# Kernel tuning notes

Measured on AMD Instinct MI355X. Metric: run time of the kernel, lower is better.

## Reference

```python
import jax, jax.numpy as jnp
import numpy as np

DIM = 512
NUM_HEADS = 8
HEAD_DIM = DIM // NUM_HEADS
GAMMA = 1.0


def setup_inputs() -> dict:
    key = jax.random.key(0)
    ks = jax.random.split(key, 10)
    B, S = 2, 2048
    x_real = jax.random.normal(ks[0], (B, S, DIM), dtype=jnp.float32)
    x_imag = jax.random.normal(ks[1], (B, S, DIM), dtype=jnp.float32)
    def xavier(k, fan_in, fan_out):
        lim = float(np.sqrt(6.0 / (fan_in + fan_out)))
        return jax.random.uniform(k, (fan_in, fan_out), jnp.float32, -lim, lim)
    # torch Linear(in,out): weight [out,in]; we store transposed [in,out]
    Wq = xavier(ks[2], 2 * DIM, DIM); bq = jnp.zeros((DIM,), jnp.float32)
    Wk = xavier(ks[3], 2 * DIM, DIM); bk = jnp.zeros((DIM,), jnp.float32)
    Wv = xavier(ks[4], 2 * DIM, DIM); bv = jnp.zeros((DIM,), jnp.float32)
    Wo = xavier(ks[5], DIM, 2 * DIM); bo = jnp.zeros((2 * DIM,), jnp.float32)
    return {"x_real": x_real, "x_imag": x_imag, "Wq": Wq, "bq": bq,
            "Wk": Wk, "bk": bk, "Wv": Wv, "bv": bv, "Wo": Wo, "bo": bo}


def reference(x_real, x_imag, Wq, bq, Wk, bk, Wv, bv, Wo, bo):
    B, S, _ = x_real.shape
    real_embed = jnp.concatenate([x_real, x_imag], axis=-1)  # [B,S,2*dim]
    def proj(W, b):
        y = real_embed @ W + b                               # [B,S,dim]
        return y.reshape(B, S, NUM_HEADS, HEAD_DIM).transpose(0, 2, 1, 3)  # [B,H,S,d]
    Q = proj(Wq, bq)
    K = proj(Wk, bk)
    V = proj(Wv, bv)
    # softmax over head_dim is broadcast-invariant, so the Bhattacharyya
    # coefficient sum_d sqrt(p_i[d]*q_j[d]) factorizes into a matmul.
    sp = jnp.sqrt(jax.nn.softmax(Q, axis=-1))  # [B,H,S,d]
    sq = jnp.sqrt(jax.nn.softmax(K, axis=-1))  # [B,H,S,d]
    bc = jnp.einsum('bhid,bhjd->bhij', sp, sq)  # Bhattacharyya coeff [B,H,S,S]
    bc = jnp.clip(bc, -1.0, 1.0)
    dist = jnp.arccos(bc)
    attn = jax.nn.softmax(-GAMMA * dist * dist, axis=-1)  # [B,H,S,S]
    attended = jnp.einsum('bhij,bhjd->bhid', attn, V)
    attended = attended.transpose(0, 2, 1, 3).reshape(B, S, DIM)
    out = attended @ Wo + bo  # [B,S,2*dim] = concat(real_out, imag_out)
    return out
```

## Files before the change

kernel.cpp:

```cpp
#include <hip/hip_runtime.h>
#include <math.h>


typedef __attribute__((ext_vector_type(8))) short short8;
typedef __attribute__((ext_vector_type(4))) float f32x4;

#define MFMA(a, b, c) __builtin_amdgcn_mfma_f32_16x16x32_bf16((a), (b), (c), 0, 0, 0)

static __device__ __forceinline__ short f2bf(float f) {
    unsigned u = __float_as_uint(f);
    u += 0x7fffu + ((u >> 16) & 1u);
    return (short)(u >> 16);
}

__global__ __launch_bounds__(256) void convert_x(
    const float* __restrict__ xr, const float* __restrict__ xi,
    short* __restrict__ xb)
{
    int idx = blockIdx.x * 256 + threadIdx.x;
    int e = idx << 2;
    int m = e >> 10, k = e & 1023;
    const float* src = (k < 512) ? xr : xi;
    float4 t = *(const float4*)(src + (size_t)m * 512 + (k & 511));
    unsigned lo = (unsigned short)f2bf(t.x) | ((unsigned)(unsigned short)f2bf(t.y) << 16);
    unsigned hi = (unsigned short)f2bf(t.z) | ((unsigned)(unsigned short)f2bf(t.w) << 16);
    uint2 o; o.x = lo; o.y = hi;
    *(uint2*)(xb + e) = o;
}

__global__ __launch_bounds__(256) void transpose_w(
    const float* __restrict__ Wq, const float* __restrict__ Wk,
    const float* __restrict__ Wv, const float* __restrict__ Wo,
    short* __restrict__ wqt, short* __restrict__ wkt,
    short* __restrict__ wvt, short* __restrict__ wot)
{
    __shared__ float t[32][33];
    const int z = blockIdx.z;
    const float* src = (z == 0) ? Wq : (z == 1) ? Wk : (z == 2) ? Wv : Wo;
    short* dst = (z == 0) ? wqt : (z == 1) ? wkt : (z == 2) ? wvt : wot;
    const int K = (z < 3) ? 1024 : 512;
    const int N = (z < 3) ? 512 : 1024;
    const int n0 = blockIdx.x << 5, k0 = blockIdx.y << 5;
    if (n0 >= N || k0 >= K) return;
    const int tx = threadIdx.x & 31, ty = threadIdx.x >> 5;
    #pragma unroll
    for (int i = 0; i < 4; ++i)
        t[ty + 8 * i][tx] = src[(size_t)(k0 + ty + 8 * i) * N + n0 + tx];
    __syncthreads();
    #pragma unroll
    for (int i = 0; i < 4; ++i)
        dst[(size_t)(n0 + ty + 8 * i) * K + k0 + tx] = f2bf(t[tx][ty + 8 * i]);
}

__global__ __launch_bounds__(128) void qkv_mfma(
    const short* __restrict__ xb,
    const short* __restrict__ wqt, const short* __restrict__ wkt,
    const short* __restrict__ wvt,
    const float* __restrict__ bq, const float* __restrict__ bk,
    const float* __restrict__ bv,
    short* __restrict__ sp, short* __restrict__ sq, short* __restrict__ vt)
{
    __shared__ short vbuf[2][64 * 72];
    const int iwb = blockIdx.x;
    const int iw = iwb >> 3;
    const int h  = iwb & 7;
    const int tid = threadIdx.x;
    const int w = tid >> 6, lane = tid & 63;
    const int l = lane & 15, quad = lane >> 4;
    const int m0 = blockIdx.y * 128 + w * 64;

    const short* wt   = (iw == 0) ? wqt : (iw == 1) ? wkt : wvt;
    const float* bias = (iw == 0) ? bq  : (iw == 1) ? bk  : bv;
    short* dst        = (iw == 0) ? sp  : (iw == 1) ? sq  : vt;

    const short* ap[4];
    const short* bp[4];
    #pragma unroll
    for (int i = 0; i < 4; ++i)
        ap[i] = xb + (size_t)(m0 + i * 16 + l) * 1024 + quad * 8;
    #pragma unroll
    for (int j = 0; j < 4; ++j)
        bp[j] = wt + (size_t)(h * 64 + j * 16 + l) * 1024 + quad * 8;

    const f32x4 z4 = {0.f, 0.f, 0.f, 0.f};
    f32x4 acc[4][4];
    #pragma unroll
    for (int i = 0; i < 4; ++i)
        #pragma unroll
        for (int j = 0; j < 4; ++j) acc[i][j] = z4;

    short8 Af[4], Bf[4], Ag[4], Bg[4];
    #pragma unroll
    for (int i = 0; i < 4; ++i) { Af[i] = *(const short8*)ap[i]; Bf[i] = *(const short8*)bp[i]; }

    #pragma unroll 1
    for (int kc = 0; kc < 32; kc += 2) {
        const int ko1 = (kc + 1) * 32;
        #pragma unroll
        for (int i = 0; i < 4; ++i) {
            Ag[i] = *(const short8*)(ap[i] + ko1);
            Bg[i] = *(const short8*)(bp[i] + ko1);
        }
        #pragma unroll
        for (int i = 0; i < 4; ++i)
            #pragma unroll
            for (int j = 0; j < 4; ++j)
                acc[i][j] = MFMA(Af[i], Bf[j], acc[i][j]);
        const int ko2 = (kc + 2 < 32) ? (kc + 2) * 32 : 0;
        #pragma unroll
        for (int i = 0; i < 4; ++i) {
            Af[i] = *(const short8*)(ap[i] + ko2);
            Bf[i] = *(const short8*)(bp[i] + ko2);
        }
        #pragma unroll
        for (int i = 0; i < 4; ++i)
            #pragma unroll
            for (int j = 0; j < 4; ++j)
                acc[i][j] = MFMA(Ag[i], Bg[j], acc[i][j]);
    }

    float bcol[4];
    #pragma unroll
    for (int nt = 0; nt < 4; ++nt) bcol[nt] = bias[h * 64 + nt * 16 + l];

    #pragma unroll
    for (int i = 0; i < 4; ++i) {
        #pragma unroll
        for (int reg = 0; reg < 4; ++reg) {
            const int sg = m0 + i * 16 + quad * 4 + reg;
            const int b = sg >> 11, s = sg & 2047;
            float v[4];
            #pragma unroll
            for (int nt = 0; nt < 4; ++nt) v[nt] = acc[i][nt][reg] + bcol[nt];
            if (iw < 2) {
                float mx = fmaxf(fmaxf(v[0], v[1]), fmaxf(v[2], v[3]));
                #pragma unroll
                for (int msk = 1; msk < 16; msk <<= 1) mx = fmaxf(mx, __shfl_xor(mx, msk));
                float e[4], ssum = 0.f;
                #pragma unroll
                for (int nt = 0; nt < 4; ++nt) { e[nt] = __expf(v[nt] - mx); ssum += e[nt]; }
                #pragma unroll
                for (int msk = 1; msk < 16; msk <<= 1) ssum += __shfl_xor(ssum, msk);
                float inv = 1.0f / ssum;
                short* o = dst + ((size_t)(b * 8 + h) * 2048 + s) * 64 + l;
                #pragma unroll
                for (int nt = 0; nt < 4; ++nt)
                    o[nt * 16] = f2bf(sqrtf(e[nt] * inv));
            } else {
                const int sl = i * 16 + quad * 4 + reg;
                #pragma unroll
                for (int nt = 0; nt < 4; ++nt)
                    vbuf[w][(nt * 16 + l) * 72 + sl] = f2bf(v[nt]);
            }
        }
    }

    if (iw == 2) {
        const int d = lane;
        const short* row = &vbuf[w][d * 72];
        const int b = m0 >> 11, s0 = m0 & 2047;
        short* gp = vt + ((size_t)(b * 8 + h) * 64 + d) * 2048 + s0;
        #pragma unroll
        for (int r = 0; r < 8; ++r)
            *(short8*)(gp + r * 8) = *(const short8*)(row + r * 8);
    }
}

__global__ __launch_bounds__(256, 4) void attn_mfma(
    const short* __restrict__ sp, const short* __restrict__ sq,
    const short* __restrict__ vt, short* __restrict__ attB)
{
    __shared__ short sqT[2][64 * 72];
    __shared__ short vtT[2][64 * 72];
    __shared__ short Pb[4][16 * 72];
    __shared__ float denB[4][16];
    const int bh = blockIdx.y;
    const int m0 = blockIdx.x << 6;
    const int tid = threadIdx.x;
    const int w = tid >> 6, lane = tid & 63;
    const int l = lane & 15, quad = lane >> 4;

    const short* spB = sp + (size_t)bh * 2048 * 64;
    const short* sqB = sq + (size_t)bh * 2048 * 64;
    const short* vtB = vt + (size_t)bh * 64 * 2048;

    const short* apr = spB + (size_t)(m0 + w * 16 + l) * 64 + quad * 8;
    short8 aq0 = *(const short8*)(apr);
    short8 aq1 = *(const short8*)(apr + 32);

    const int srow = tid >> 2;
    const int scol = (tid & 3) * 16;
    const short* sqG = sqB + (size_t)srow * 64 + scol;
    const short* vtG = vtB + (size_t)srow * 2048 + scol;
    const int ldsOff = srow * 72 + scol;

    {
        short8 a0 = *(const short8*)(sqG);
        short8 a1 = *(const short8*)(sqG + 8);
        short8 b0 = *(const short8*)(vtG);
        short8 b1 = *(const short8*)(vtG + 8);
        *(short8*)(&sqT[0][ldsOff])     = a0;
        *(short8*)(&sqT[0][ldsOff + 8]) = a1;
        *(short8*)(&vtT[0][ldsOff])     = b0;
        *(short8*)(&vtT[0][ldsOff + 8]) = b1;
    }
    __syncthreads();

    const f32x4 z4 = {0.f, 0.f, 0.f, 0.f};
    f32x4 acc[4] = {z4, z4, z4, z4};
    float den = 0.f;
    short* Pw = &Pb[w][0];

    #pragma unroll 1
    for (int jt = 0; jt < 32; ++jt) {
        const int cb = jt & 1, nb = cb ^ 1;
        const int j0n = ((jt + 1) & 31) << 6;
        short8 na0 = *(const short8*)(sqG + (size_t)j0n * 64);
        short8 na1 = *(const short8*)(sqG + (size_t)j0n * 64 + 8);
        short8 nb0 = *(const short8*)(vtG + j0n);
        short8 nb1 = *(const short8*)(vtG + j0n + 8);

        const short* sqL = &sqT[cb][0];
        #pragma unroll
        for (int nt = 0; nt < 4; ++nt) {
            const short* ar = sqL + (nt * 16 + l) * 72 + quad * 8;
            short8 sa0 = *(const short8*)(ar);
            short8 sa1 = *(const short8*)(ar + 32);
            f32x4 p = MFMA(sa0, aq0, z4);
            p = MFMA(sa1, aq1, p);
            float wv[4];
            #pragma unroll
            for (int reg = 0; reg < 4; ++reg) {
                float u = fmaxf(1.0f - p[reg], 0.0f);
                float t = 0.000922f;
                t = fmaf(t, u, 0.00152228f);
                t = fmaf(t, u, 0.00384801f);
                t = fmaf(t, u, 0.01015873f);
                t = fmaf(t, u, 0.02857143f);
                t = fmaf(t, u, 0.08888889f);
                t = fmaf(t, u, 0.33333333f);
                t = fmaf(t, u, 2.0f);
                float e = __expf(-u * t);
                wv[reg] = e;
                den += e;
            }
            uint2 pk;
            pk.x = (__float_as_uint(wv[0]) >> 16) | (__float_as_uint(wv[1]) & 0xffff0000u);
            pk.y = (__float_as_uint(wv[2]) >> 16) | (__float_as_uint(wv[3]) & 0xffff0000u);
            *(uint2*)(&Pw[l * 72 + nt * 16 + quad * 4]) = pk;
        }

        const short* pr = Pw + l * 72 + quad * 8;
        short8 pa0 = *(const short8*)(pr);
        short8 pa1 = *(const short8*)(pr + 32);
        const short* vL = &vtT[cb][0];
        #pragma unroll
        for (int t4 = 0; t4 < 4; ++t4) {
            const short* vr = vL + (t4 * 16 + l) * 72 + quad * 8;
            short8 vb0 = *(const short8*)(vr);
            short8 vb1 = *(const short8*)(vr + 32);
            acc[t4] = MFMA(pa0, vb0, acc[t4]);
            acc[t4] = MFMA(pa1, vb1, acc[t4]);
        }

        *(short8*)(&sqT[nb][ldsOff])     = na0;
        *(short8*)(&sqT[nb][ldsOff + 8]) = na1;
        *(short8*)(&vtT[nb][ldsOff])     = nb0;
        *(short8*)(&vtT[nb][ldsOff + 8]) = nb1;
        __syncthreads();
    }

    den += __shfl_xor(den, 16);
    den += __shfl_xor(den, 32);
    if (lane < 16) denB[w][l] = den;
    float invd[4];
    #pragma unroll
    for (int reg = 0; reg < 4; ++reg)
        invd[reg] = 1.0f / denB[w][quad * 4 + reg];

    const int b = bh >> 3, hh = bh & 7;
    #pragma unroll
    for (int t4 = 0; t4 < 4; ++t4)
        #pragma unroll
        for (int reg = 0; reg < 4; ++reg) {
            const int row = m0 + w * 16 + quad * 4 + reg;
            attB[((size_t)(b * 2048 + row)) * 512 + hh * 64 + t4 * 16 + l] =
                f2bf(acc[t4][reg] * invd[reg]);
        }
}

__global__ __launch_bounds__(128) void out_mfma(
    const short* __restrict__ attB, const short* __restrict__ wot,
    const float* __restrict__ bo, float* __restrict__ out)
{
    const int n0 = blockIdx.x << 6;
    const int tid = threadIdx.x;
    const int w = tid >> 6, lane = tid & 63;
    const int l = lane & 15, quad = lane >> 4;
    const int m0 = blockIdx.y * 128 + w * 64;

    const short* ap[4];
    const short* bp[4];
    #pragma unroll
    for (int i = 0; i < 4; ++i)
        ap[i] = attB + (size_t)(m0 + i * 16 + l) * 512 + quad * 8;
    #pragma unroll
    for (int j = 0; j < 4; ++j)
        bp[j] = wot + (size_t)(n0 + j * 16 + l) * 512 + quad * 8;

    const f32x4 z4 = {0.f, 0.f, 0.f, 0.f};
    f32x4 acc[4][4];
    #pragma unroll
    for (int i = 0; i < 4; ++i)
        #pragma unroll
        for (int j = 0; j < 4; ++j) acc[i][j] = z4;

    short8 Af[4], Bf[4], Ag[4], Bg[4];
    #pragma unroll
    for (int i = 0; i < 4; ++i) { Af[i] = *(const short8*)ap[i]; Bf[i] = *(const short8*)bp[i]; }

    #pragma unroll 1
    for (int kc = 0; kc < 16; kc += 2) {
        const int ko1 = (kc + 1) * 32;
        #pragma unroll
        for (int i = 0; i < 4; ++i) {
            Ag[i] = *(const short8*)(ap[i] + ko1);
            Bg[i] = *(const short8*)(bp[i] + ko1);
        }
        #pragma unroll
        for (int i = 0; i < 4; ++i)
            #pragma unroll
            for (int j = 0; j < 4; ++j)
                acc[i][j] = MFMA(Af[i], Bf[j], acc[i][j]);
        const int ko2 = (kc + 2 < 16) ? (kc + 2) * 32 : 0;
        #pragma unroll
        for (int i = 0; i < 4; ++i) {
            Af[i] = *(const short8*)(ap[i] + ko2);
            Bf[i] = *(const short8*)(bp[i] + ko2);
        }
        #pragma unroll
        for (int i = 0; i < 4; ++i)
            #pragma unroll
            for (int j = 0; j < 4; ++j)
                acc[i][j] = MFMA(Ag[i], Bg[j], acc[i][j]);
    }

    #pragma unroll
    for (int i = 0; i < 4; ++i)
        #pragma unroll
        for (int reg = 0; reg < 4; ++reg) {
            const int m = m0 + i * 16 + quad * 4 + reg;
            float* o = out + (size_t)m * 1024 + n0 + l;
            #pragma unroll
            for (int nt = 0; nt < 4; ++nt)
                o[nt * 16] = acc[i][nt][reg] + bo[n0 + nt * 16 + l];
        }
}

extern "C" void kernel_launch(void* const* d_in, const int* in_sizes, int n_in,
                              void* d_out, int out_size, void* d_ws, size_t ws_size,
                              hipStream_t stream) {
    const float* xr = (const float*)d_in[0];
    const float* xi = (const float*)d_in[1];
    const float* Wq = (const float*)d_in[2];
    const float* bq = (const float*)d_in[3];
    const float* Wk = (const float*)d_in[4];
    const float* bk = (const float*)d_in[5];
    const float* Wv = (const float*)d_in[6];
    const float* bv = (const float*)d_in[7];
    const float* Wo = (const float*)d_in[8];
    const float* bo = (const float*)d_in[9];
    float* out = (float*)d_out;

    short* base = (short*)d_ws;
    short* xb   = base;
    short* wqt  = xb  + 4194304;
    short* wkt  = wqt + 524288;
    short* wvt  = wkt + 524288;
    short* wot  = wvt + 524288;
    short* spW  = wot + 524288;
    short* sqW  = spW + 2097152;
    short* vtW  = sqW + 2097152;
    short* attB = vtW + 2097152;

    hipLaunchKernelGGL(convert_x, dim3(4096), dim3(256), 0, stream, xr, xi, xb);
    hipLaunchKernelGGL(transpose_w, dim3(32, 32, 4), dim3(256), 0, stream,
                       Wq, Wk, Wv, Wo, wqt, wkt, wvt, wot);
    hipLaunchKernelGGL(qkv_mfma, dim3(24, 32), dim3(128), 0, stream,
                       xb, wqt, wkt, wvt, bq, bk, bv, spW, sqW, vtW);
    hipLaunchKernelGGL(attn_mfma, dim3(32, 16), dim3(256), 0, stream,
                       spW, sqW, vtW, attB);
    hipLaunchKernelGGL(out_mfma, dim3(16, 32), dim3(128), 0, stream,
                       attB, wot, bo, out);
}
```

Baseline: 214.6 us.

## Stage QKV and output GEMM tiles in LDS via async global-to-LDS loads

The QKV projection and output projection GEMMs now stage A and B tiles in double-buffered shared memory, filled with global_load_lds direct copies, instead of having each wave read its fragments straight from global memory. The QKV kernel runs 256 threads on 128x128 tiles over the concatenated Wq/Wk/Wv (wqt, wkt, wvt are assumed contiguous), and V is written transposed directly as 4-element packed stores without the LDS transpose buffer. The goal is to raise operand reuse across waves and cut redundant global traffic. In exchange it adds a __syncthreads per k-step, and the LDS tile layout is unpadded, which may cause bank conflicts.

```diff
diff --git a/kernel.cpp b/kernel.cpp
--- a/kernel.cpp
+++ b/kernel.cpp
@@ -3,6 +3,7 @@
 
 
 typedef __attribute__((ext_vector_type(8))) short short8;
+typedef __attribute__((ext_vector_type(4))) short bf16x4;
 typedef __attribute__((ext_vector_type(4))) float f32x4;
 
 #define MFMA(a, b, c) __builtin_amdgcn_mfma_f32_16x16x32_bf16((a), (b), (c), 0, 0, 0)
@@ -11,6 +12,12 @@
     unsigned u = __float_as_uint(f);
     u += 0x7fffu + ((u >> 16) & 1u);
     return (short)(u >> 16);
+}
+
+static __device__ __forceinline__ void gld_lds16(const short* g, short* l) {
+    __builtin_amdgcn_global_load_lds(
+        (const __attribute__((address_space(1))) unsigned int*)g,
+        (__attribute__((address_space(3))) unsigned int*)l, 16, 0, 0);
 }
 
 __global__ __launch_bounds__(256) void convert_x(
@@ -52,35 +59,28 @@
         dst[(size_t)(n0 + ty + 8 * i) * K + k0 + tx] = f2bf(t[tx][ty + 8 * i]);
 }
 
-__global__ __launch_bounds__(128) void qkv_mfma(
-    const short* __restrict__ xb,
-    const short* __restrict__ wqt, const short* __restrict__ wkt,
-    const short* __restrict__ wvt,
+__global__ __launch_bounds__(256, 3) void qkv_mfma(
+    const short* __restrict__ xb, const short* __restrict__ wcat,
     const float* __restrict__ bq, const float* __restrict__ bk,
     const float* __restrict__ bv,
     short* __restrict__ sp, short* __restrict__ sq, short* __restrict__ vt)
 {
-    __shared__ short vbuf[2][64 * 72];
-    const int iwb = blockIdx.x;
-    const int iw = iwb >> 3;
-    const int h  = iwb & 7;
+    __shared__ short As[2][128 * 32];
+    __shared__ short Bs[2][128 * 32];
+    const int jb = blockIdx.x;
+    const int m0 = blockIdx.y << 7;
     const int tid = threadIdx.x;
     const int w = tid >> 6, lane = tid & 63;
     const int l = lane & 15, quad = lane >> 4;
-    const int m0 = blockIdx.y * 128 + w * 64;
-
-    const short* wt   = (iw == 0) ? wqt : (iw == 1) ? wkt : wvt;
-    const float* bias = (iw == 0) ? bq  : (iw == 1) ? bk  : bv;
-    short* dst        = (iw == 0) ? sp  : (iw == 1) ? sq  : vt;
-
-    const short* ap[4];
-    const short* bp[4];
-    #pragma unroll
-    for (int i = 0; i < 4; ++i)
-        ap[i] = xb + (size_t)(m0 + i * 16 + l) * 1024 + quad * 8;
-    #pragma unroll
-    for (int j = 0; j < 4; ++j)
-        bp[j] = wt + (size_t)(h * 64 + j * 16 + l) * 1024 + quad * 8;
+
+    const short* gA = xb   + (size_t)(m0        + (w << 4) + (lane >> 2)) * 1024 + ((lane & 3) << 3);
+    const short* gB = wcat + (size_t)((jb << 7) + (w << 4) + (lane >> 2)) * 1024 + ((lane & 3) << 3);
+
+    gld_lds16(gA,             &As[0][w << 9]);
+    gld_lds16(gA + 64 * 1024, &As[0][(w + 4) << 9]);
+    gld_lds16(gB,             &Bs[0][w << 9]);
+    gld_lds16(gB + 64 * 1024, &Bs[0][(w + 4) << 9]);
+    __syncthreads();
 
     const f32x4 z4 = {0.f, 0.f, 0.f, 0.f};
     f32x4 acc[4][4];
@@ -89,50 +89,53 @@
         #pragma unroll
         for (int j = 0; j < 4; ++j) acc[i][j] = z4;
 
-    short8 Af[4], Bf[4], Ag[4], Bg[4];
-    #pragma unroll
-    for (int i = 0; i < 4; ++i) { Af[i] = *(const short8*)ap[i]; Bf[i] = *(const short8*)bp[i]; }
-
-    #pragma unroll 1
-    for (int kc = 0; kc < 32; kc += 2) {
-        const int ko1 = (kc + 1) * 32;
-        #pragma unroll
-        for (int i = 0; i < 4; ++i) {
-            Ag[i] = *(const short8*)(ap[i] + ko1);
-            Bg[i] = *(const short8*)(bp[i] + ko1);
-        }
+    const int rsel = (w >> 1) << 6;
+    const int csel = (w & 1) << 6;
+
+    for (int kt = 0; kt < 32; ++kt) {
+        const int cb = kt & 1, nb = cb ^ 1;
+        if (kt < 31) {
+            const int k0 = (kt + 1) << 5;
+            gld_lds16(gA + k0,             &As[nb][w << 9]);
+            gld_lds16(gA + k0 + 64 * 1024, &As[nb][(w + 4) << 9]);
+            gld_lds16(gB + k0,             &Bs[nb][w << 9]);
+            gld_lds16(gB + k0 + 64 * 1024, &Bs[nb][(w + 4) << 9]);
+        }
+        const short* Al = &As[cb][rsel << 5];
+        const short* Bl = &Bs[cb][csel << 5];
+        short8 af[4], bfr[4];
+        #pragma unroll
+        for (int i = 0; i < 4; ++i)
+            af[i] = *(const short8*)(Al + (((i << 4) + l) << 5) + (quad << 3));
+        #pragma unroll
+        for (int j = 0; j < 4; ++j)
+            bfr[j] = *(const short8*)(Bl + (((j << 4) + l) << 5) + (quad << 3));
         #pragma unroll
         for (int i = 0; i < 4; ++i)
             #pragma unroll
             for (int j = 0; j < 4; ++j)
-                acc[i][j] = MFMA(Af[i], Bf[j], acc[i][j]);
-        const int ko2 = (kc + 2 < 32) ? (kc + 2) * 32 : 0;
+                acc[i][j] = MFMA(af[i], bfr[j], acc[i][j]);
+        __syncthreads();
+    }
+
+    const int op = jb >> 2;
+    const int h  = ((jb & 3) << 1) | (w & 1);
+
+    if (op < 2) {
+        short* dst = (op == 0) ? sp : sq;
+        const float* bias = (op == 0) ? bq : bk;
+        float bcol[4];
+        #pragma unroll
+        for (int nt = 0; nt < 4; ++nt) bcol[nt] = bias[(h << 6) + (nt << 4) + l];
         #pragma unroll
         for (int i = 0; i < 4; ++i) {
-            Af[i] = *(const short8*)(ap[i] + ko2);
-            Bf[i] = *(const short8*)(bp[i] + ko2);
-        }
-        #pragma unroll
-        for (int i = 0; i < 4; ++i)
             #pragma unroll
-            for (int j = 0; j < 4; ++j)
-                acc[i][j] = MFMA(Ag[i], Bg[j], acc[i][j]);
-    }
-
-    float bcol[4];
-    #pragma unroll
-    for (int nt = 0; nt < 4; ++nt) bcol[nt] = bias[h * 64 + nt * 16 + l];
-
-    #pragma unroll
-    for (int i = 0; i < 4; ++i) {
-        #pragma unroll
-        for (int reg = 0; reg < 4; ++reg) {
-            const int sg = m0 + i * 16 + quad * 4 + reg;
-            const int b = sg >> 11, s = sg & 2047;
-            float v[4];
-            #pragma unroll
-            for (int nt = 0; nt < 4; ++nt) v[nt] = acc[i][nt][reg] + bcol[nt];
-            if (iw < 2) {
+            for (int reg = 0; reg < 4; ++reg) {
+                const int r = m0 + rsel + (i << 4) + (quad << 2) + reg;
+                const int b = r >> 11, s = r & 2047;
+                float v[4];
+                #pragma unroll
+                for (int nt = 0; nt < 4; ++nt) v[nt] = acc[i][nt][reg] + bcol[nt];
                 float mx = fmaxf(fmaxf(v[0], v[1]), fmaxf(v[2], v[3]));
                 #pragma unroll
                 for (int msk = 1; msk < 16; msk <<= 1) mx = fmaxf(mx, __shfl_xor(mx, msk));
@@ -142,27 +145,30 @@
                 #pragma unroll
                 for (int msk = 1; msk < 16; msk <<= 1) ssum += __shfl_xor(ssum, msk);
                 float inv = 1.0f / ssum;
-                short* o = dst + ((size_t)(b * 8 + h) * 2048 + s) * 64 + l;
+                short* o = dst + ((size_t)((b << 3) + h) * 2048 + s) * 64 + l;
                 #pragma unroll
                 for (int nt = 0; nt < 4; ++nt)
-                    o[nt * 16] = f2bf(sqrtf(e[nt] * inv));
-            } else {
-                const int sl = i * 16 + quad * 4 + reg;
-                #pragma unroll
-                for (int nt = 0; nt < 4; ++nt)
-                    vbuf[w][(nt * 16 + l) * 72 + sl] = f2bf(v[nt]);
+                    o[nt << 4] = f2bf(sqrtf(e[nt] * inv));
             }
         }
-    }
-
-    if (iw == 2) {
-        const int d = lane;
-        const short* row = &vbuf[w][d * 72];
-        const int b = m0 >> 11, s0 = m0 & 2047;
-        short* gp = vt + ((size_t)(b * 8 + h) * 64 + d) * 2048 + s0;
-        #pragma unroll
-        for (int r = 0; r < 8; ++r)
-            *(short8*)(gp + r * 8) = *(const short8*)(row + r * 8);
+    } else {
+        float bcol[4];
+        #pragma unroll
+        for (int nt = 0; nt < 4; ++nt) bcol[nt] = bv[(h << 6) + (nt << 4) + l];
+        #pragma unroll
+        for (int i = 0; i < 4; ++i) {
+            const int sb = m0 + rsel + (i << 4) + (quad << 2);
+            const int b = sb >> 11, s = sb & 2047;
+            #pragma unroll
+            for (int nt = 0; nt < 4; ++nt) {
+                const int d = (nt << 4) + l;
+                bf16x4 pk;
+                #pragma unroll
+                for (int reg = 0; reg < 4; ++reg)
+                    pk[reg] = f2bf(acc[i][nt][reg] + bcol[nt]);
+                *(bf16x4*)(vt + ((size_t)((b << 3) + h) * 64 + d) * 2048 + s) = pk;
+            }
+        }
     }
 }
 
@@ -289,71 +295,71 @@
         }
 }
 
-__global__ __launch_bounds__(128) void out_mfma(
+__global__ __launch_bounds__(256, 3) void out_mfma(
     const short* __restrict__ attB, const short* __restrict__ wot,
     const float* __restrict__ bo, float* __restrict__ out)
 {
-    const int n0 = blockIdx.x << 6;
+    __shared__ short As[2][128 * 32];
+    __shared__ short Bs[2][64 * 32];
+    const int nb0 = blockIdx.x << 6;
+    const int m0 = blockIdx.y << 7;
     const int tid = threadIdx.x;
     const int w = tid >> 6, lane = tid & 63;
     const int l = lane & 15, quad = lane >> 4;
-    const int m0 = blockIdx.y * 128 + w * 64;
-
-    const short* ap[4];
-    const short* bp[4];
+
+    const short* gA = attB + (size_t)(m0  + (w << 4) + (lane >> 2)) * 512 + ((lane & 3) << 3);
+    const short* gB = wot  + (size_t)(nb0 + (w << 4) + (lane >> 2)) * 512 + ((lane & 3) << 3);
+
+    gld_lds16(gA,            &As[0][w << 9]);
+    gld_lds16(gA + 64 * 512, &As[0][(w + 4) << 9]);
+    gld_lds16(gB,            &Bs[0][w << 9]);
+    __syncthreads();
+
+    const f32x4 z4 = {0.f, 0.f, 0.f, 0.f};
+    f32x4 acc[4][2];
+    #pragma unroll
+    for (int i = 0; i < 4; ++i) { acc[i][0] = z4; acc[i][1] = z4; }
+
+    const int rsel = (w >> 1) << 6;
+    const int csel = (w & 1) << 5;
+
+    for (int kt = 0; kt < 16; ++kt) {
+        const int cb = kt & 1, nbuf = cb ^ 1;
+        if (kt < 15) {
+            const int k0 = (kt + 1) << 5;
+            gld_lds16(gA + k0,            &As[nbuf][w << 9]);
+            gld_lds16(gA + k0 + 64 * 512, &As[nbuf][(w + 4) << 9]);
+            gld_lds16(gB + k0,            &Bs[nbuf][w << 9]);
+        }
+        const short* Al = &As[cb][rsel << 5];
+        const short* Bl = &Bs[cb][csel << 5];
+        short8 af[4], bfr[2];
+        #pragma unroll
+        for (int i = 0; i < 4; ++i)
+            af[i] = *(const short8*)(Al + (((i << 4) + l) << 5) + (quad << 3));
+        #pragma unroll
+        for (int j = 0; j < 2; ++j)
+            bfr[j] = *(const short8*)(Bl + (((j << 4) + l) << 5) + (quad << 3));
+        #pragma unroll
+        for (int i = 0; i < 4; ++i) {
+            acc[i][0] = MFMA(af[i], bfr[0], acc[i][0]);
+            acc[i][1] = MFMA(af[i], bfr[1], acc[i][1]);
+        }
+        __syncthreads();
+    }
+
+    const int n0 = nb0 + csel;
+    float bcol[2];
+    bcol[0] = bo[n0 + l];
+    bcol[1] = bo[n0 + 16 + l];
     #pragma unroll
     for (int i = 0; i < 4; ++i)
-        ap[i] = attB + (size_t)(m0 + i * 16 + l) * 512 + quad * 8;
-    #pragma unroll
-    for (int j = 0; j < 4; ++j)
-        bp[j] = wot + (size_t)(n0 + j * 16 + l) * 512 + quad * 8;
-
-    const f32x4 z4 = {0.f, 0.f, 0.f, 0.f};
-    f32x4 acc[4][4];
-    #pragma unroll
-    for (int i = 0; i < 4; ++i)
-        #pragma unroll
-        for (int j = 0; j < 4; ++j) acc[i][j] = z4;
-
-    short8 Af[4], Bf[4], Ag[4], Bg[4];
-    #pragma unroll
-    for (int i = 0; i < 4; ++i) { Af[i] = *(const short8*)ap[i]; Bf[i] = *(const short8*)bp[i]; }
-
-    #pragma unroll 1
-    for (int kc = 0; kc < 16; kc += 2) {
-        const int ko1 = (kc + 1) * 32;
-        #pragma unroll
-        for (int i = 0; i < 4; ++i) {
-            Ag[i] = *(const short8*)(ap[i] + ko1);
-            Bg[i] = *(const short8*)(bp[i] + ko1);
-        }
-        #pragma unroll
-        for (int i = 0; i < 4; ++i)
-            #pragma unroll
-            for (int j = 0; j < 4; ++j)
-                acc[i][j] = MFMA(Af[i], Bf[j], acc[i][j]);
-        const int ko2 = (kc + 2 < 16) ? (kc + 2) * 32 : 0;
-        #pragma unroll
-        for (int i = 0; i < 4; ++i) {
-            Af[i] = *(const short8*)(ap[i] + ko2);
-            Bf[i] = *(const short8*)(bp[i] + ko2);
-        }
-        #pragma unroll
-        for (int i = 0; i < 4; ++i)
-            #pragma unroll
-            for (int j = 0; j < 4; ++j)
-                acc[i][j] = MFMA(Ag[i], Bg[j], acc[i][j]);
-    }
-
-    #pragma unroll
-    for (int i = 0; i < 4; ++i)
         #pragma unroll
         for (int reg = 0; reg < 4; ++reg) {
-            const int m = m0 + i * 16 + quad * 4 + reg;
+            const int m = m0 + rsel + (i << 4) + (quad << 2) + reg;
             float* o = out + (size_t)m * 1024 + n0 + l;
-            #pragma unroll
-            for (int nt = 0; nt < 4; ++nt)
-                o[nt * 16] = acc[i][nt][reg] + bo[n0 + nt * 16 + l];
+            o[0]  = acc[i][0][reg] + bcol[0];
+            o[16] = acc[i][1][reg] + bcol[1];
         }
 }
 
@@ -386,10 +392,10 @@
     hipLaunchKernelGGL(convert_x, dim3(4096), dim3(256), 0, stream, xr, xi, xb);
     hipLaunchKernelGGL(transpose_w, dim3(32, 32, 4), dim3(256), 0, stream,
                        Wq, Wk, Wv, Wo, wqt, wkt, wvt, wot);
-    hipLaunchKernelGGL(qkv_mfma, dim3(24, 32), dim3(128), 0, stream,
-                       xb, wqt, wkt, wvt, bq, bk, bv, spW, sqW, vtW);
+    hipLaunchKernelGGL(qkv_mfma, dim3(12, 32), dim3(256), 0, stream,
+                       xb, wqt, bq, bk, bv, spW, sqW, vtW);
     hipLaunchKernelGGL(attn_mfma, dim3(32, 16), dim3(256), 0, stream,
                        spW, sqW, vtW, attB);
-    hipLaunchKernelGGL(out_mfma, dim3(16, 32), dim3(128), 0, stream,
+    hipLaunchKernelGGL(out_mfma, dim3(16, 32), dim3(256), 0, stream,
                        attB, wot, bo, out);
 }
```

Result: faster. 184.7 us (-13.9%).
